# Performance work log

Hardware: AMD Instinct MI355X
Metric: run time of the kernel (lower is better)

The kernel has to match this reference:

```python
import jax, jax.numpy as jnp
import numpy as np

EPS_NORM = 1e-12  # torch F.normalize eps


def _resize_bilinear_ac(x, H, W):
    # Bilinear resize with align_corners=True on NCHW tensor x.
    h, w = x.shape[-2], x.shape[-1]
    ys = jnp.linspace(0.0, h - 1.0, H)
    xs = jnp.linspace(0.0, w - 1.0, W)
    y0 = jnp.floor(ys).astype(jnp.int32); y1 = jnp.minimum(y0 + 1, h - 1)
    x0 = jnp.floor(xs).astype(jnp.int32); x1 = jnp.minimum(x0 + 1, w - 1)
    wy = (ys - y0).astype(x.dtype)[None, None, :, None]
    wx = (xs - x0).astype(x.dtype)
    rows = x[:, :, y0, :] * (1 - wy) + x[:, :, y1, :] * wy  # (B,C,H,w)
    return rows[:, :, :, x0] * (1 - wx) + rows[:, :, :, x1] * wx  # (B,C,H,W)


def _icc(p, b):
    # p: (b, 19, hw) row-stochastic over hw.
    # M[i, j] = KLDiv(input=p_i, target=p_j, batchmean) = (1/b) * sum p_j*(log p_j - p_i)
    # NOTE: original code passes probabilities (not log-probs) as KLDiv input; kept faithful.
    E = jnp.sum(p * jnp.log(p), axis=(0, 2))            # (19,) sum_b,k p log p
    G = jnp.einsum('bik,bjk->ij', p, p)                  # (19,19) sum_b,k p_i p_j
    M = (E[None, :] - G) / b
    sym = jnp.triu(M) + jnp.triu(M, 1).T                 # loop writes value for i<=j to both [i,j],[j,i]
    nrm = jnp.maximum(jnp.linalg.norm(sym, axis=1, keepdims=True), EPS_NORM)
    return sym / nrm                                     # F.normalize(dim=1)


def reference(s_out, t_out, t_logit, s_logit, conv_w, conv_b):
    T = 1.0  # temperature
    # --- pi_loss ---
    B, C, H, W = t_out.shape
    s1 = _resize_bilinear_ac(s_out, H, W)
    s1 = jnp.einsum('bchw,oc->bohw', s1, conv_w[:, :, 0, 0]) + conv_b[None, :, None, None]
    log_ps = jax.nn.log_softmax(s1 / T, axis=1)
    pt = jax.nn.softmax(t_out / T, axis=1)
    # torch KLDivLoss() default reduction='mean' (mean over ALL elements)
    pi_loss = jnp.mean(pt * (jnp.log(pt) - log_ps))
    # --- lo_loss ---
    b, n, h, w = s_logit.shape
    tl = _resize_bilinear_ac(t_logit, h, w)
    s = jax.nn.softmax(s_logit.reshape(b, n, h * w) / T, axis=2)
    t = jax.nn.softmax(tl.reshape(b, n, h * w) / T, axis=2)
    ICCS = _icc(s, b)
    ICCT = _icc(t, b)
    lo_loss = jnp.sum((ICCS - ICCT) ** 2)
    return pi_loss, lo_loss


def setup_inputs() -> dict:
    key = jax.random.key(0)
    k = jax.random.split(key, 6)
    return {
        's_out': jax.random.normal(k[0], (8, 128, 33, 33), jnp.float32),
        't_out': jax.random.normal(k[1], (8, 768, 65, 65), jnp.float32),
        't_logit': jax.random.normal(k[2], (8, 19, 65, 65), jnp.float32),
        's_logit': jax.random.normal(k[3], (8, 19, 129, 129), jnp.float32),
        'conv_w': jax.random.normal(k[4], (768, 128, 1, 1), jnp.float32) * 0.05,
        'conv_b': jax.random.normal(k[5], (768,), jnp.float32) * 0.05,
    }
```

## Files before the change

### kernel.cpp

```cpp
#include <hip/hip_runtime.h>
#include <math.h>

#define WS_E0   0
#define WS_E1   19
#define WS_G0   64
#define WS_G1   448
#define WS_Z    1152
#define WS_WBF  2048
#define WS_PIX  51200
#define PIXHALF 137216

typedef __bf16 bf16x8 __attribute__((ext_vector_type(8)));
typedef float  f32x4  __attribute__((ext_vector_type(4)));

__global__ void k_init(const float* __restrict__ conv_w, float* __restrict__ ws,
                       float* __restrict__ out) {
    int gid = blockIdx.x * 256 + threadIdx.x;
    __bf16* Wb = (__bf16*)(ws + WS_WBF);
    #pragma unroll
    for (int j = 0; j < 6; j++) {
        int idx = gid + j * 16384;
        Wb[idx] = (__bf16)conv_w[idx];
    }
    if (blockIdx.x == 0) {
        for (int k = (int)threadIdx.x; k < 2048; k += 256) ws[k] = 0.f;
        if (threadIdx.x < 2) out[threadIdx.x] = 0.f;
    }
}

__device__ __forceinline__ float t_resized(const float* __restrict__ Trow, int k) {
    int y = k / 129, x = k - y * 129;
    int y0 = y >> 1, x0 = x >> 1;
    int y1 = y0 + (y & 1), x1 = x0 + (x & 1);
    float fy = 0.5f * (float)(y & 1), fx = 0.5f * (float)(x & 1);
    float v00 = Trow[y0 * 65 + x0], v01 = Trow[y0 * 65 + x1];
    float v10 = Trow[y1 * 65 + x0], v11 = Trow[y1 * 65 + x1];
    float r0 = v00 + fx * (v01 - v00);
    float r1 = v10 + fx * (v11 - v10);
    return r0 + fy * (r1 - r0);
}

__launch_bounds__(256, 2)
__global__ void k_main(const float* __restrict__ s_out, const float* __restrict__ t_out,
                       const float* __restrict__ bias,
                       const float* __restrict__ s_logit, const float* __restrict__ t_logit,
                       float* __restrict__ ws, float* __restrict__ out) {
    __shared__ __align__(16) char lds[17408];
    const int tid = threadIdx.x;
    const int bx  = blockIdx.x;

    if (bx < 1072) {
        __bf16* xs    = (__bf16*)lds;
        float*  tbase = (float*)lds;
        float*  scr   = (float*)lds;

        const int half = bx & 1;
        const int bt   = bx >> 1;
        const int b    = bt / 67;
        const int tile = bt - b * 67;
        const int hw0  = tile * 64;
        const bool tail = (tile == 66);

        {
            const float* Sb = s_out + b * 128 * 1089;
            #pragma unroll
            for (int ii = 0; ii < 32; ii++) {
                int idx = tid + ii * 256;
                int c = idx >> 6, px = idx & 63;
                int hw = hw0 + px;
                float v = 0.f;
                if (hw < 4225) {
                    int h = hw / 65, w = hw - h * 65;
                    int y0 = h >> 1, x0 = w >> 1;
                    int y1 = y0 + (h & 1), x1 = x0 + (w & 1);
                    float wy = 0.5f * (float)(h & 1), wx = 0.5f * (float)(w & 1);
                    const float* Sc = Sb + c * 1089;
                    float v00 = Sc[y0 * 33 + x0], v01 = Sc[y0 * 33 + x1];
                    float v10 = Sc[y1 * 33 + x0], v11 = Sc[y1 * 33 + x1];
                    float r0 = v00 + wx * (v01 - v00);
                    float r1 = v10 + wx * (v11 - v10);
                    v = r0 + wy * (r1 - r0);
                }
                xs[px * 136 + c] = (__bf16)v;
            }
        }
        __syncthreads();

        const int l = tid & 63, wv = tid >> 6, q = l >> 4, n = l & 15;

        bf16x8 bfrag[4][4];
        #pragma unroll
        for (int pt = 0; pt < 4; pt++)
            #pragma unroll
            for (int kf = 0; kf < 4; kf++)
                bfrag[pt][kf] = *(const bf16x8*)&xs[(pt * 16 + n) * 136 + kf * 32 + q * 8];
        __syncthreads();

        const __bf16* Wbf = (const __bf16*)(ws + WS_WBF);
        float* tst = tbase + wv * 1088;

        float Zt[4], St[4], Dd[4], Zs[4];
        #pragma unroll
        for (int pt = 0; pt < 4; pt++) { Zt[pt] = 0.f; St[pt] = 0.f; Dd[pt] = 0.f; Zs[pt] = 0.f; }

        float4 t4[4];
        auto load_t = [&](int ch, float4* dst) {
            const float* tb = t_out + (size_t)(b * 768 + ch * 64 + wv * 16) * 4225;
            #pragma unroll
            for (int ii = 0; ii < 4; ii++) {
                int lin = ii * 64 + l;
                int row = lin >> 4, p4 = lin & 15;
                if (!tail) {
                    dst[ii] = *(const float4*)(tb + row * 4225 + hw0 + p4 * 4);
                } else {
                    const float* rr = tb + row * 4225;
                    int b0 = hw0 + p4 * 4;
                    float4 v;
                    v.x = rr[min(b0 + 0, 4224)];
                    v.y = rr[min(b0 + 1, 4224)];
                    v.z = rr[min(b0 + 2, 4224)];
                    v.w = rr[min(b0 + 3, 4224)];
                    dst[ii] = v;
                }
            }
        };
        load_t(half * 6, t4);

        for (int c6 = 0; c6 < 6; c6++) {
            const int ch  = half * 6 + c6;
            const int ob  = ch * 64 + wv * 16;
            const int o_r = ob + q * 4;

            #pragma unroll
            for (int ii = 0; ii < 4; ii++) {
                int lin = ii * 64 + l;
                int row = lin >> 4, p4 = lin & 15;
                *(float4*)(tst + row * 68 + p4 * 4) = t4[ii];
            }

            bf16x8 afrag[4];
            const __bf16* Wr = Wbf + (size_t)(ob + n) * 128 + q * 8;
            #pragma unroll
            for (int kf = 0; kf < 4; kf++)
                afrag[kf] = *(const bf16x8*)(Wr + kf * 32);
            f32x4 bq = *(const f32x4*)&bias[o_r];

            float4 t4n[4];
            const bool pf = (c6 < 5);
            if (pf) load_t(ch + 1, t4n);

            f32x4 acc[4];
            #pragma unroll
            for (int pt = 0; pt < 4; pt++) {
                f32x4 a0 = {0.f, 0.f, 0.f, 0.f};
                #pragma unroll
                for (int kf = 0; kf < 4; kf++)
                    a0 = __builtin_amdgcn_mfma_f32_16x16x32_bf16(afrag[kf], bfrag[pt][kf], a0, 0, 0, 0);
                acc[pt] = a0;
            }

            #pragma unroll
            for (int pt = 0; pt < 4; pt++) {
                #pragma unroll
                for (int r = 0; r < 4; r++) {
                    float tv  = tst[(q * 4 + r) * 68 + pt * 16 + n];
                    float s1v = acc[pt][r] + bq[r];
                    float e   = __expf(tv);
                    Zt[pt] += e;
                    St[pt]  = fmaf(e, tv,  St[pt]);
                    Dd[pt]  = fmaf(e, s1v, Dd[pt]);
                    Zs[pt] += __expf(s1v);
                }
            }

            if (pf) {
                #pragma unroll
                for (int ii = 0; ii < 4; ii++) t4[ii] = t4n[ii];
            }
        }

        __syncthreads();
        {
            int part = wv * 4 + q;
            #pragma unroll
            for (int pt = 0; pt < 4; pt++) {
                f32x4 v = {Zt[pt], St[pt], Dd[pt], Zs[pt]};
                *(f32x4*)&scr[(pt * 16 + n) * 68 + part * 4] = v;
            }
        }
        __syncthreads();
        if (tid < 64) {
            float Z = 0.f, S = 0.f, D = 0.f, Z2 = 0.f;
            #pragma unroll
            for (int p = 0; p < 16; p++) {
                const float* s4 = &scr[tid * 68 + p * 4];
                Z += s4[0]; S += s4[1]; D += s4[2]; Z2 += s4[3];
            }
            f32x4 v = {Z, S, D, Z2};
            *(f32x4*)&ws[WS_PIX + half * PIXHALF + ((size_t)b * 4288 + tile * 64 + tid) * 4] = v;
        }
    } else {
        float* red = (float*)lds;
        int row  = bx - 1072;
        int side = (row >= 152) ? 1 : 0;
        int r    = side ? row - 152 : row;
        const float* src = side ? (t_logit + r * 4225) : (s_logit + r * 16641);

        float z = 0.f, s = 0.f;
        for (int k = tid; k < 16641; k += 256) {
            float v = side ? t_resized(src, k) : src[k];
            float e = __expf(v);
            z += e;
            s = fmaf(e, v, s);
        }
        for (int off = 32; off > 0; off >>= 1) { z += __shfl_down(z, off); s += __shfl_down(s, off); }
        if ((tid & 63) == 0) { red[tid >> 6] = z; red[4 + (tid >> 6)] = s; }
        __syncthreads();
        if (tid == 0) {
            float Z = red[0] + red[1] + red[2] + red[3];
            float S = red[4] + red[5] + red[6] + red[7];
            ws[WS_Z + row] = Z;
            atomicAdd(&ws[(side ? WS_E1 : WS_E0) + (r % 19)], S / Z - logf(Z));
        }
    }
}

#define KT 512
#define KP 516
__global__ void k_mid(const float* __restrict__ s_logit, const float* __restrict__ t_logit,
                      float* __restrict__ ws, float* __restrict__ out) {
    __shared__ __align__(16) char lds[39296];
    const int tid = threadIdx.x;
    const int bx  = blockIdx.x;

    if (bx < 528) {
        float* pbuf  = (float*)lds;
        float* rowiz = (float*)(lds + 39216);
        int side = (bx >= 264) ? 1 : 0;
        int rm   = side ? bx - 264 : bx;
        int b = rm / 33, kt = rm - b * 33;
        int k0 = kt * KT;

        if (tid < 19) rowiz[tid] = 1.0f / ws[WS_Z + side * 152 + b * 19 + tid];
        __syncthreads();

        for (int i = 0; i < 19; i++) {
            const float* src = side ? (t_logit + (b * 19 + i) * 4225) : (s_logit + (b * 19 + i) * 16641);
            float iz = rowiz[i];
            for (int kl = tid; kl < KT; kl += 256) {
                int k = k0 + kl;
                float p = 0.f;
                if (k < 16641) {
                    float v = side ? t_resized(src, k) : src[k];
                    p = __expf(v) * iz;
                }
                pbuf[i * KP + kl] = p;
            }
        }
        __syncthreads();

        if (tid < 190) {
            int t = tid, i = 0;
            while (t >= 19 - i) { t -= 19 - i; i++; }
            int j = i + t;
            const float* pi_ = &pbuf[i * KP];
            const float* pj_ = &pbuf[j * KP];
            float g = 0.f;
            #pragma unroll 4
            for (int kl = 0; kl < KT; kl += 4) {
                float4 a = *(const float4*)&pi_[kl];
                float4 c = *(const float4*)&pj_[kl];
                g = fmaf(a.x, c.x, g); g = fmaf(a.y, c.y, g);
                g = fmaf(a.z, c.z, g); g = fmaf(a.w, c.w, g);
            }
            atomicAdd(&ws[(side ? WS_G1 : WS_G0) + i * 19 + j], g);
        }
    } else {
        float* red = (float*)lds;
        int gp = (bx - 528) * 256 + tid;
        int b  = gp / 4288;
        int tp = gp - b * 4288;
        f32x4 a = *(const f32x4*)&ws[WS_PIX + (size_t)gp * 4];
        f32x4 c = *(const f32x4*)&ws[WS_PIX + PIXHALF + (size_t)gp * 4];
        float Z = a[0] + c[0], S = a[1] + c[1], D = a[2] + c[2], Z2 = a[3] + c[3];
        float contrib = (tp < 4225) ? ((S - D) / Z - logf(Z) + logf(Z2)) : 0.f;
        for (int off = 32; off > 0; off >>= 1) contrib += __shfl_down(contrib, off);
        if ((tid & 63) == 0) red[tid >> 6] = contrib;
        __syncthreads();
        if (tid == 0)
            atomicAdd(out, (red[0] + red[1] + red[2] + red[3]) * (1.0f / 25958400.0f));
    }
}

__global__ void k_final(const float* __restrict__ ws, float* __restrict__ out) {
    __shared__ float Ms[361], Mt[361], ns[19], nt[19];
    __shared__ float red[8];
    int tid = threadIdx.x;
    if (tid < 361) {
        int i = tid / 19, j = tid - i * 19;
        int lo = min(i, j), hi = max(i, j);
        Ms[tid] = (ws[WS_E0 + hi] - ws[WS_G0 + lo * 19 + hi]) * 0.125f;
        Mt[tid] = (ws[WS_E1 + hi] - ws[WS_G1 + lo * 19 + hi]) * 0.125f;
    }
    __syncthreads();
    if (tid < 19) {
        float as = 0.f, at = 0.f;
        for (int j = 0; j < 19; j++) {
            as = fmaf(Ms[tid * 19 + j], Ms[tid * 19 + j], as);
            at = fmaf(Mt[tid * 19 + j], Mt[tid * 19 + j], at);
        }
        ns[tid] = fmaxf(sqrtf(as), 1e-12f);
        nt[tid] = fmaxf(sqrtf(at), 1e-12f);
    }
    __syncthreads();
    float d = 0.f;
    if (tid < 361) {
        int i = tid / 19;
        float v = Ms[tid] / ns[i] - Mt[tid] / nt[i];
        d = v * v;
    }
    for (int off = 32; off > 0; off >>= 1) d += __shfl_down(d, off);
    if ((tid & 63) == 0) red[tid >> 6] = d;
    __syncthreads();
    if (tid == 0) out[1] = red[0] + red[1] + red[2] + red[3] + red[4] + red[5];
}

extern "C" void kernel_launch(void* const* d_in, const int* in_sizes, int n_in,
                              void* d_out, int out_size, void* d_ws, size_t ws_size,
                              hipStream_t stream) {
    const float* s_out   = (const float*)d_in[0];
    const float* t_out   = (const float*)d_in[1];
    const float* t_logit = (const float*)d_in[2];
    const float* s_logit = (const float*)d_in[3];
    const float* conv_w  = (const float*)d_in[4];
    const float* conv_b  = (const float*)d_in[5];
    float* out = (float*)d_out;
    float* ws  = (float*)d_ws;

    k_init<<<dim3(64), dim3(256), 0, stream>>>(conv_w, ws, out);
    k_main<<<dim3(1376), dim3(256), 0, stream>>>(s_out, t_out, conv_b, s_logit, t_logit, ws, out);
    k_mid<<<dim3(662), dim3(256), 0, stream>>>(s_logit, t_logit, ws, out);
    k_final<<<dim3(1), dim3(384), 0, stream>>>(ws, out);
}
```

Measured before the change: 276.7 us.

## Split channels into quarters, stream t_out directly into LDS, reduce partials atomically

The main kernel now splits the 768 output channels four ways instead of two, so it launches twice as many pixel-tile blocks. Each block issues all of its t_out loads up front with global_load_lds, writing straight into a larger LDS buffer. This replaces the register-staged double-buffer prefetch loop. Per-pixel partial sums are combined with atomicAdd into a single buffer that k_init now zeroes, removing the second half-buffer read in the finishing pass. The costs are more LDS per block, which limits residency, more atomics, and losing the overlap between each chunk's loads and its MFMA compute.

```diff
diff --git a/kernel.cpp b/kernel.cpp
--- a/kernel.cpp
+++ b/kernel.cpp
@@ -8,23 +8,28 @@
 #define WS_Z    1152
 #define WS_WBF  2048
 #define WS_PIX  51200
-#define PIXHALF 137216
 
 typedef __bf16 bf16x8 __attribute__((ext_vector_type(8)));
 typedef float  f32x4  __attribute__((ext_vector_type(4)));
 
+typedef const __attribute__((address_space(1))) unsigned int guint;
+typedef       __attribute__((address_space(3))) unsigned int luint;
+
 __global__ void k_init(const float* __restrict__ conv_w, float* __restrict__ ws,
                        float* __restrict__ out) {
-    int gid = blockIdx.x * 256 + threadIdx.x;
-    __bf16* Wb = (__bf16*)(ws + WS_WBF);
-    #pragma unroll
-    for (int j = 0; j < 6; j++) {
-        int idx = gid + j * 16384;
-        Wb[idx] = (__bf16)conv_w[idx];
-    }
-    if (blockIdx.x == 0) {
-        for (int k = (int)threadIdx.x; k < 2048; k += 256) ws[k] = 0.f;
-        if (threadIdx.x < 2) out[threadIdx.x] = 0.f;
+    const int bx = blockIdx.x, tid = threadIdx.x;
+    ws[WS_PIX + bx * 256 + tid] = 0.f;
+    if (bx < 96) {
+        __bf16* Wb = (__bf16*)(ws + WS_WBF);
+        #pragma unroll
+        for (int j = 0; j < 4; j++) {
+            int idx = bx * 1024 + j * 256 + tid;
+            Wb[idx] = (__bf16)conv_w[idx];
+        }
+    }
+    if (bx == 96) {
+        for (int k = tid; k < 2048; k += 256) ws[k] = 0.f;
+        if (tid < 2) out[tid] = 0.f;
     }
 }
 
@@ -45,17 +50,16 @@
                        const float* __restrict__ bias,
                        const float* __restrict__ s_logit, const float* __restrict__ t_logit,
                        float* __restrict__ ws, float* __restrict__ out) {
-    __shared__ __align__(16) char lds[17408];
+    __shared__ __align__(16) char lds[69632];
     const int tid = threadIdx.x;
     const int bx  = blockIdx.x;
 
-    if (bx < 1072) {
-        __bf16* xs    = (__bf16*)lds;
-        float*  tbase = (float*)lds;
-        float*  scr   = (float*)lds;
-
-        const int half = bx & 1;
-        const int bt   = bx >> 1;
+    if (bx < 2144) {
+        __bf16* xs  = (__bf16*)lds;
+        float*  scr = (float*)lds;
+
+        const int half = bx & 3;
+        const int bt   = bx >> 2;
         const int b    = bt / 67;
         const int tile = bt - b * 67;
         const int hw0  = tile * 64;
@@ -97,74 +101,53 @@
         __syncthreads();
 
         const __bf16* Wbf = (const __bf16*)(ws + WS_WBF);
-        float* tst = tbase + wv * 1088;
-
+        bf16x8 afr[3][4];
+        f32x4  bq[3];
+        #pragma unroll
+        for (int c = 0; c < 3; c++) {
+            const int ob = (half * 3 + c) * 64 + wv * 16;
+            const __bf16* Wr = Wbf + (size_t)(ob + n) * 128 + q * 8;
+            #pragma unroll
+            for (int kf = 0; kf < 4; kf++) afr[c][kf] = *(const bf16x8*)(Wr + kf * 32);
+            bq[c] = *(const f32x4*)&bias[ob + q * 4];
+        }
+
+        char* tw = lds + 17408 + wv * 13056;
+        const int hw0c = tail ? 4161 : hw0;
+        #pragma unroll
+        for (int c = 0; c < 3; c++) {
+            const int ob = (half * 3 + c) * 64 + wv * 16;
+            const float* gb = t_out + (size_t)(b * 768 + ob) * 4225 + hw0c;
+            #pragma unroll
+            for (int r = 0; r < 16; r++) {
+                __builtin_amdgcn_global_load_lds((guint*)(gb + (size_t)r * 4225 + l),
+                                                 (luint*)(tw + c * 4352 + r * 272), 4, 0, 0);
+            }
+        }
+        asm volatile("s_waitcnt vmcnt(0)" ::: "memory");
+
+        const float* tstf = (const float*)tw;
         float Zt[4], St[4], Dd[4], Zs[4];
         #pragma unroll
         for (int pt = 0; pt < 4; pt++) { Zt[pt] = 0.f; St[pt] = 0.f; Dd[pt] = 0.f; Zs[pt] = 0.f; }
 
-        float4 t4[4];
-        auto load_t = [&](int ch, float4* dst) {
-            const float* tb = t_out + (size_t)(b * 768 + ch * 64 + wv * 16) * 4225;
-            #pragma unroll
-            for (int ii = 0; ii < 4; ii++) {
-                int lin = ii * 64 + l;
-                int row = lin >> 4, p4 = lin & 15;
-                if (!tail) {
-                    dst[ii] = *(const float4*)(tb + row * 4225 + hw0 + p4 * 4);
-                } else {
-                    const float* rr = tb + row * 4225;
-                    int b0 = hw0 + p4 * 4;
-                    float4 v;
-                    v.x = rr[min(b0 + 0, 4224)];
-                    v.y = rr[min(b0 + 1, 4224)];
-                    v.z = rr[min(b0 + 2, 4224)];
-                    v.w = rr[min(b0 + 3, 4224)];
-                    dst[ii] = v;
-                }
-            }
-        };
-        load_t(half * 6, t4);
-
-        for (int c6 = 0; c6 < 6; c6++) {
-            const int ch  = half * 6 + c6;
-            const int ob  = ch * 64 + wv * 16;
-            const int o_r = ob + q * 4;
-
-            #pragma unroll
-            for (int ii = 0; ii < 4; ii++) {
-                int lin = ii * 64 + l;
-                int row = lin >> 4, p4 = lin & 15;
-                *(float4*)(tst + row * 68 + p4 * 4) = t4[ii];
-            }
-
-            bf16x8 afrag[4];
-            const __bf16* Wr = Wbf + (size_t)(ob + n) * 128 + q * 8;
-            #pragma unroll
-            for (int kf = 0; kf < 4; kf++)
-                afrag[kf] = *(const bf16x8*)(Wr + kf * 32);
-            f32x4 bq = *(const f32x4*)&bias[o_r];
-
-            float4 t4n[4];
-            const bool pf = (c6 < 5);
-            if (pf) load_t(ch + 1, t4n);
-
+        #pragma unroll
+        for (int c = 0; c < 3; c++) {
             f32x4 acc[4];
             #pragma unroll
             for (int pt = 0; pt < 4; pt++) {
                 f32x4 a0 = {0.f, 0.f, 0.f, 0.f};
                 #pragma unroll
                 for (int kf = 0; kf < 4; kf++)
-                    a0 = __builtin_amdgcn_mfma_f32_16x16x32_bf16(afrag[kf], bfrag[pt][kf], a0, 0, 0, 0);
+                    a0 = __builtin_amdgcn_mfma_f32_16x16x32_bf16(afr[c][kf], bfrag[pt][kf], a0, 0, 0, 0);
                 acc[pt] = a0;
             }
-
             #pragma unroll
             for (int pt = 0; pt < 4; pt++) {
                 #pragma unroll
                 for (int r = 0; r < 4; r++) {
-                    float tv  = tst[(q * 4 + r) * 68 + pt * 16 + n];
-                    float s1v = acc[pt][r] + bq[r];
+                    float tv  = tstf[c * 1088 + (q * 4 + r) * 68 + (tail ? 63 : pt * 16 + n)];
+                    float s1v = acc[pt][r] + bq[c][r];
                     float e   = __expf(tv);
                     Zt[pt] += e;
                     St[pt]  = fmaf(e, tv,  St[pt]);
@@ -172,11 +155,6 @@
                     Zs[pt] += __expf(s1v);
                 }
             }
-
-            if (pf) {
-                #pragma unroll
-                for (int ii = 0; ii < 4; ii++) t4[ii] = t4n[ii];
-            }
         }
 
         __syncthreads();
@@ -196,12 +174,15 @@
                 const float* s4 = &scr[tid * 68 + p * 4];
                 Z += s4[0]; S += s4[1]; D += s4[2]; Z2 += s4[3];
             }
-            f32x4 v = {Z, S, D, Z2};
-            *(f32x4*)&ws[WS_PIX + half * PIXHALF + ((size_t)b * 4288 + tile * 64 + tid) * 4] = v;
+            float* dst = &ws[WS_PIX + ((size_t)b * 4288 + tile * 64 + tid) * 4];
+            atomicAdd(dst + 0, Z);
+            atomicAdd(dst + 1, S);
+            atomicAdd(dst + 2, D);
+            atomicAdd(dst + 3, Z2);
         }
     } else {
         float* red = (float*)lds;
-        int row  = bx - 1072;
+        int row  = bx - 2144;
         int side = (row >= 152) ? 1 : 0;
         int r    = side ? row - 152 : row;
         const float* src = side ? (t_logit + r * 4225) : (s_logit + r * 16641);
@@ -281,8 +262,7 @@
         int b  = gp / 4288;
         int tp = gp - b * 4288;
         f32x4 a = *(const f32x4*)&ws[WS_PIX + (size_t)gp * 4];
-        f32x4 c = *(const f32x4*)&ws[WS_PIX + PIXHALF + (size_t)gp * 4];
-        float Z = a[0] + c[0], S = a[1] + c[1], D = a[2] + c[2], Z2 = a[3] + c[3];
+        float Z = a[0], S = a[1], D = a[2], Z2 = a[3];
         float contrib = (tp < 4225) ? ((S - D) / Z - logf(Z) + logf(Z2)) : 0.f;
         for (int off = 32; off > 0; off >>= 1) contrib += __shfl_down(contrib, off);
         if ((tid & 63) == 0) red[tid >> 6] = contrib;
@@ -337,8 +317,8 @@
     float* out = (float*)d_out;
     float* ws  = (float*)d_ws;
 
-    k_init<<<dim3(64), dim3(256), 0, stream>>>(conv_w, ws, out);
-    k_main<<<dim3(1376), dim3(256), 0, stream>>>(s_out, t_out, conv_b, s_logit, t_logit, ws, out);
+    k_init<<<dim3(536), dim3(256), 0, stream>>>(conv_w, ws, out);
+    k_main<<<dim3(2448), dim3(256), 0, stream>>>(s_out, t_out, conv_b, s_logit, t_logit, ws, out);
     k_mid<<<dim3(662), dim3(256), 0, stream>>>(s_logit, t_logit, ws, out);
     k_final<<<dim3(1), dim3(384), 0, stream>>>(ws, out);
 }
```

New measurement: 300.5 us. +8.6%, slower.

## Precompute resized bf16 student features in prep kernel and peel tail pixel

Applied to the files above, without the earlier changes.

Moves the bilinear upsampling of s_out into a separate prep kernel that writes a bf16 pixel-major buffer to workspace, so the main kernel loads MFMA B fragments directly from global memory instead of rebuilding them in LDS for each half. The single leftover pixel (index 4224) is handled by dedicated per-batch blocks with a scalar dot product, which removes the tail-clamped loads and tail tiles. The t_out prefetch becomes double-buffered two channels ahead with a fully unrolled loop. In exchange there is an extra workspace round trip of about 8.6MB and more register pressure.

```diff
diff --git a/kernel.cpp b/kernel.cpp
--- a/kernel.cpp
+++ b/kernel.cpp
@@ -7,24 +7,48 @@
 #define WS_G1   448
 #define WS_Z    1152
 #define WS_WBF  2048
-#define WS_PIX  51200
-#define PIXHALF 137216
+#define WS_XRES 51200
+#define WS_PIX  2213888
 
 typedef __bf16 bf16x8 __attribute__((ext_vector_type(8)));
 typedef float  f32x4  __attribute__((ext_vector_type(4)));
 
-__global__ void k_init(const float* __restrict__ conv_w, float* __restrict__ ws,
-                       float* __restrict__ out) {
-    int gid = blockIdx.x * 256 + threadIdx.x;
-    __bf16* Wb = (__bf16*)(ws + WS_WBF);
-    #pragma unroll
-    for (int j = 0; j < 6; j++) {
-        int idx = gid + j * 16384;
-        Wb[idx] = (__bf16)conv_w[idx];
-    }
-    if (blockIdx.x == 0) {
-        for (int k = (int)threadIdx.x; k < 2048; k += 256) ws[k] = 0.f;
-        if (threadIdx.x < 2) out[threadIdx.x] = 0.f;
+__global__ void k_prep(const float* __restrict__ s_out, const float* __restrict__ conv_w,
+                       float* __restrict__ ws, float* __restrict__ out) {
+    const int bx = blockIdx.x, tid = threadIdx.x;
+    if (bx < 264) {
+        const int b     = bx / 33;
+        const int strip = bx - b * 33;
+        const int px0   = strip * 128;
+        const float* Sb = s_out + (size_t)b * 128 * 1089;
+        __bf16* Xb = (__bf16*)(ws + WS_XRES) + (size_t)b * 4224 * 128;
+        #pragma unroll
+        for (int ii = 0; ii < 64; ii++) {
+            int id2 = tid + ii * 256;
+            int c = id2 & 127, px = id2 >> 7;
+            int hw = px0 + px;
+            int h = hw / 65, w = hw - h * 65;
+            int y0 = h >> 1, x0 = w >> 1;
+            int y1 = y0 + (h & 1), x1 = x0 + (w & 1);
+            float wy = 0.5f * (float)(h & 1), wx = 0.5f * (float)(w & 1);
+            const float* Sc = Sb + c * 1089;
+            float v00 = Sc[y0 * 33 + x0], v01 = Sc[y0 * 33 + x1];
+            float v10 = Sc[y1 * 33 + x0], v11 = Sc[y1 * 33 + x1];
+            float r0 = v00 + wx * (v01 - v00);
+            float r1 = v10 + wx * (v11 - v10);
+            Xb[(size_t)hw * 128 + c] = (__bf16)(r0 + wy * (r1 - r0));
+        }
+    } else if (bx < 360) {
+        const int bb = bx - 264;
+        __bf16* Wb = (__bf16*)(ws + WS_WBF);
+        #pragma unroll
+        for (int j = 0; j < 4; j++) {
+            int idx = bb * 1024 + j * 256 + tid;
+            Wb[idx] = (__bf16)conv_w[idx];
+        }
+    } else {
+        for (int k = tid; k < 2048; k += 256) ws[k] = 0.f;
+        if (tid < 2) out[tid] = 0.f;
     }
 }
 
@@ -41,60 +65,34 @@
 }
 
 __launch_bounds__(256, 2)
-__global__ void k_main(const float* __restrict__ s_out, const float* __restrict__ t_out,
-                       const float* __restrict__ bias,
-                       const float* __restrict__ s_logit, const float* __restrict__ t_logit,
-                       float* __restrict__ ws, float* __restrict__ out) {
+__global__ void k_pi(const float* __restrict__ s_out, const float* __restrict__ t_out,
+                     const float* __restrict__ conv_w, const float* __restrict__ bias,
+                     const float* __restrict__ s_logit, const float* __restrict__ t_logit,
+                     float* __restrict__ ws, float* __restrict__ out) {
     __shared__ __align__(16) char lds[17408];
     const int tid = threadIdx.x;
     const int bx  = blockIdx.x;
 
-    if (bx < 1072) {
-        __bf16* xs    = (__bf16*)lds;
-        float*  tbase = (float*)lds;
-        float*  scr   = (float*)lds;
-
-        const int half = bx & 1;
-        const int bt   = bx >> 1;
-        const int b    = bt / 67;
-        const int tile = bt - b * 67;
+    if (bx >= 304 && bx < 1360) {
+        float* tbase = (float*)lds;
+        float* scr   = (float*)lds;
+
+        const int idx  = bx - 304;
+        const int half = idx & 1;
+        const int bt   = idx >> 1;
+        const int b    = bt / 66;
+        const int tile = bt - b * 66;
         const int hw0  = tile * 64;
-        const bool tail = (tile == 66);
-
-        {
-            const float* Sb = s_out + b * 128 * 1089;
-            #pragma unroll
-            for (int ii = 0; ii < 32; ii++) {
-                int idx = tid + ii * 256;
-                int c = idx >> 6, px = idx & 63;
-                int hw = hw0 + px;
-                float v = 0.f;
-                if (hw < 4225) {
-                    int h = hw / 65, w = hw - h * 65;
-                    int y0 = h >> 1, x0 = w >> 1;
-                    int y1 = y0 + (h & 1), x1 = x0 + (w & 1);
-                    float wy = 0.5f * (float)(h & 1), wx = 0.5f * (float)(w & 1);
-                    const float* Sc = Sb + c * 1089;
-                    float v00 = Sc[y0 * 33 + x0], v01 = Sc[y0 * 33 + x1];
-                    float v10 = Sc[y1 * 33 + x0], v11 = Sc[y1 * 33 + x1];
-                    float r0 = v00 + wx * (v01 - v00);
-                    float r1 = v10 + wx * (v11 - v10);
-                    v = r0 + wy * (r1 - r0);
-                }
-                xs[px * 136 + c] = (__bf16)v;
-            }
-        }
-        __syncthreads();
 
         const int l = tid & 63, wv = tid >> 6, q = l >> 4, n = l & 15;
 
+        const __bf16* Xb = (const __bf16*)(ws + WS_XRES) + (size_t)b * 4224 * 128;
         bf16x8 bfrag[4][4];
         #pragma unroll
         for (int pt = 0; pt < 4; pt++)
             #pragma unroll
             for (int kf = 0; kf < 4; kf++)
-                bfrag[pt][kf] = *(const bf16x8*)&xs[(pt * 16 + n) * 136 + kf * 32 + q * 8];
-        __syncthreads();
+                bfrag[pt][kf] = *(const bf16x8*)(Xb + (size_t)(hw0 + pt * 16 + n) * 128 + kf * 32 + q * 8);
 
         const __bf16* Wbf = (const __bf16*)(ws + WS_WBF);
         float* tst = tbase + wv * 1088;
@@ -103,51 +101,38 @@
         #pragma unroll
         for (int pt = 0; pt < 4; pt++) { Zt[pt] = 0.f; St[pt] = 0.f; Dd[pt] = 0.f; Zs[pt] = 0.f; }
 
-        float4 t4[4];
+        float4 t4[2][4];
         auto load_t = [&](int ch, float4* dst) {
             const float* tb = t_out + (size_t)(b * 768 + ch * 64 + wv * 16) * 4225;
             #pragma unroll
             for (int ii = 0; ii < 4; ii++) {
                 int lin = ii * 64 + l;
                 int row = lin >> 4, p4 = lin & 15;
-                if (!tail) {
-                    dst[ii] = *(const float4*)(tb + row * 4225 + hw0 + p4 * 4);
-                } else {
-                    const float* rr = tb + row * 4225;
-                    int b0 = hw0 + p4 * 4;
-                    float4 v;
-                    v.x = rr[min(b0 + 0, 4224)];
-                    v.y = rr[min(b0 + 1, 4224)];
-                    v.z = rr[min(b0 + 2, 4224)];
-                    v.w = rr[min(b0 + 3, 4224)];
-                    dst[ii] = v;
-                }
+                dst[ii] = *(const float4*)(tb + (size_t)row * 4225 + hw0 + p4 * 4);
             }
         };
-        load_t(half * 6, t4);
-
+        load_t(half * 6 + 0, t4[0]);
+        load_t(half * 6 + 1, t4[1]);
+
+        #pragma unroll
         for (int c6 = 0; c6 < 6; c6++) {
+            const int cur = c6 & 1;
             const int ch  = half * 6 + c6;
             const int ob  = ch * 64 + wv * 16;
-            const int o_r = ob + q * 4;
 
             #pragma unroll
             for (int ii = 0; ii < 4; ii++) {
                 int lin = ii * 64 + l;
                 int row = lin >> 4, p4 = lin & 15;
-                *(float4*)(tst + row * 68 + p4 * 4) = t4[ii];
-            }
+                *(float4*)(tst + row * 68 + p4 * 4) = t4[cur][ii];
+            }
+            if (c6 < 4) load_t(ch + 2, t4[cur]);
 
             bf16x8 afrag[4];
             const __bf16* Wr = Wbf + (size_t)(ob + n) * 128 + q * 8;
             #pragma unroll
-            for (int kf = 0; kf < 4; kf++)
-                afrag[kf] = *(const bf16x8*)(Wr + kf * 32);
-            f32x4 bq = *(const f32x4*)&bias[o_r];
-
-            float4 t4n[4];
-            const bool pf = (c6 < 5);
-            if (pf) load_t(ch + 1, t4n);
+            for (int kf = 0; kf < 4; kf++) afrag[kf] = *(const bf16x8*)(Wr + kf * 32);
+            f32x4 bq = *(const f32x4*)&bias[ob + q * 4];
 
             f32x4 acc[4];
             #pragma unroll
@@ -172,11 +157,6 @@
                     Zs[pt] += __expf(s1v);
                 }
             }
-
-            if (pf) {
-                #pragma unroll
-                for (int ii = 0; ii < 4; ii++) t4[ii] = t4n[ii];
-            }
         }
 
         __syncthreads();
@@ -197,11 +177,11 @@
                 Z += s4[0]; S += s4[1]; D += s4[2]; Z2 += s4[3];
             }
             f32x4 v = {Z, S, D, Z2};
-            *(f32x4*)&ws[WS_PIX + half * PIXHALF + ((size_t)b * 4288 + tile * 64 + tid) * 4] = v;
-        }
-    } else {
+            *(f32x4*)&ws[WS_PIX + ((size_t)half * 33792 + (size_t)b * 4224 + hw0 + tid) * 4] = v;
+        }
+    } else if (bx < 304) {
         float* red = (float*)lds;
-        int row  = bx - 1072;
+        int row  = bx;
         int side = (row >= 152) ? 1 : 0;
         int r    = side ? row - 152 : row;
         const float* src = side ? (t_logit + r * 4225) : (s_logit + r * 16641);
@@ -221,6 +201,40 @@
             float S = red[4] + red[5] + red[6] + red[7];
             ws[WS_Z + row] = Z;
             atomicAdd(&ws[(side ? WS_E1 : WS_E0) + (r % 19)], S / Z - logf(Z));
+        }
+    } else {
+        float* xc  = (float*)lds;
+        float* red = (float*)lds + 128;
+        const int b = bx - 1360;
+        if (tid < 128) xc[tid] = s_out[((size_t)b * 128 + tid) * 1089 + 1088];
+        __syncthreads();
+        float z = 0.f, s = 0.f, d = 0.f, z2 = 0.f;
+        #pragma unroll
+        for (int rep = 0; rep < 3; rep++) {
+            int o = tid + rep * 256;
+            const float* Wr = conv_w + (size_t)o * 128;
+            float s1 = bias[o];
+            for (int cc = 0; cc < 128; cc++) s1 = fmaf(Wr[cc], xc[cc], s1);
+            float tv = t_out[((size_t)(b * 768 + o)) * 4225 + 4224];
+            float e  = __expf(tv);
+            z += e; s = fmaf(e, tv, s); d = fmaf(e, s1, d); z2 += __expf(s1);
+        }
+        for (int off = 32; off > 0; off >>= 1) {
+            z += __shfl_down(z, off); s += __shfl_down(s, off);
+            d += __shfl_down(d, off); z2 += __shfl_down(z2, off);
+        }
+        if ((tid & 63) == 0) {
+            int wv = tid >> 6;
+            red[wv] = z; red[4 + wv] = s; red[8 + wv] = d; red[12 + wv] = z2;
+        }
+        __syncthreads();
+        if (tid == 0) {
+            float Z = red[0] + red[1] + red[2] + red[3];
+            float S = red[4] + red[5] + red[6] + red[7];
+            float D = red[8] + red[9] + red[10] + red[11];
+            float Z2 = red[12] + red[13] + red[14] + red[15];
+            float contrib = (S - D) / Z - logf(Z) + logf(Z2);
+            atomicAdd(out, contrib * (1.0f / 25958400.0f));
         }
     }
 }
@@ -278,12 +292,10 @@
     } else {
         float* red = (float*)lds;
         int gp = (bx - 528) * 256 + tid;
-        int b  = gp / 4288;
-        int tp = gp - b * 4288;
         f32x4 a = *(const f32x4*)&ws[WS_PIX + (size_t)gp * 4];
-        f32x4 c = *(const f32x4*)&ws[WS_PIX + PIXHALF + (size_t)gp * 4];
+        f32x4 c = *(const f32x4*)&ws[WS_PIX + ((size_t)33792 + gp) * 4];
         float Z = a[0] + c[0], S = a[1] + c[1], D = a[2] + c[2], Z2 = a[3] + c[3];
-        float contrib = (tp < 4225) ? ((S - D) / Z - logf(Z) + logf(Z2)) : 0.f;
+        float contrib = (S - D) / Z - logf(Z) + logf(Z2);
         for (int off = 32; off > 0; off >>= 1) contrib += __shfl_down(contrib, off);
         if ((tid & 63) == 0) red[tid >> 6] = contrib;
         __syncthreads();
@@ -337,8 +349,9 @@
     float* out = (float*)d_out;
     float* ws  = (float*)d_ws;
 
-    k_init<<<dim3(64), dim3(256), 0, stream>>>(conv_w, ws, out);
-    k_main<<<dim3(1376), dim3(256), 0, stream>>>(s_out, t_out, conv_b, s_logit, t_logit, ws, out);
-    k_mid<<<dim3(662), dim3(256), 0, stream>>>(s_logit, t_logit, ws, out);
+    k_prep<<<dim3(361), dim3(256), 0, stream>>>(s_out, conv_w, ws, out);
+    k_pi<<<dim3(1368), dim3(256), 0, stream>>>(s_out, t_out, conv_w, conv_b,
+                                               s_logit, t_logit, ws, out);
+    k_mid<<<dim3(660), dim3(256), 0, stream>>>(s_logit, t_logit, ws, out);
     k_final<<<dim3(1), dim3(384), 0, stream>>>(ws, out);
 }
```

After: 304.1 us. +9.9%, slower.
